# Kernel optimization log

Hardware: AMD Instinct MI355X
Metric: run time of the kernel (lower is better)

Reference implementation:

```python
import jax, jax.numpy as jnp
import numpy as np

N = 50000      # nodes
E = 800000     # edges (before self loops)
IN_D = 128
HID = 128
OUT_D = 64
HEADS = 4
FH = HID // HEADS  # per-head feature dim
NEG_SLOPE = 0.2


def setup_inputs() -> dict:
    key = jax.random.key(0)
    ks = jax.random.split(key, 16)
    s = 0.05
    inp = {
        "x": jax.random.normal(ks[0], (N, IN_D), dtype=jnp.float32),
        "edge_index": jax.random.randint(ks[1], (2, E), 0, N, dtype=jnp.int32),
        "Wi": jax.random.normal(ks[2], (IN_D, HID), dtype=jnp.float32) * s,
        "bi": jnp.zeros((HID,), dtype=jnp.float32),
        "W0": jax.random.normal(ks[3], (HID, HID), dtype=jnp.float32) * s,
        "as0": jax.random.normal(ks[4], (HEADS, FH), dtype=jnp.float32) * s,
        "ad0": jax.random.normal(ks[5], (HEADS, FH), dtype=jnp.float32) * s,
        "b0": jnp.zeros((HID,), dtype=jnp.float32),
        "W1": jax.random.normal(ks[6], (HID, HID), dtype=jnp.float32) * s,
        "as1": jax.random.normal(ks[7], (HEADS, FH), dtype=jnp.float32) * s,
        "ad1": jax.random.normal(ks[8], (HEADS, FH), dtype=jnp.float32) * s,
        "b1": jnp.zeros((HID,), dtype=jnp.float32),
        "Wo": jax.random.normal(ks[9], (HID, OUT_D), dtype=jnp.float32) * s,
        "bo": jnp.zeros((OUT_D,), dtype=jnp.float32),
    }
    return inp


def _gat_layer(h, src, dst, W, a_src, a_dst, b):
    # h: [N, HID]; src/dst: [E'] (with self loops)
    hp = (h @ W).reshape(N, HEADS, FH)               # projected per-head features
    al_s = jnp.einsum('nhf,hf->nh', hp, a_src)       # [N, H]
    al_d = jnp.einsum('nhf,hf->nh', hp, a_dst)
    e = jax.nn.leaky_relu(al_s[src] + al_d[dst], NEG_SLOPE)  # [E', H]
    # neighbor softmax over incoming edges of each dst node (stable)
    m = jax.ops.segment_max(e, dst, num_segments=N)
    m = jnp.where(jnp.isfinite(m), m, 0.0)
    num = jnp.exp(e - m[dst])
    den = jax.ops.segment_sum(num, dst, num_segments=N)
    coef = num / (den[dst] + 1e-16)                  # [E', H]
    out = jax.ops.segment_sum(coef[:, :, None] * hp[src], dst, num_segments=N)
    return out.reshape(N, HID) + b


def reference(x, edge_index, Wi, bi, W0, as0, ad0, b0, W1, as1, ad1, b1, Wo, bo):
    # add self loops (PyG GATConv default)
    loop = jnp.arange(N, dtype=edge_index.dtype)
    src = jnp.concatenate([edge_index[0], loop])
    dst = jnp.concatenate([edge_index[1], loop])

    h = jax.nn.relu(x @ Wi + bi)
    # layer 0 (dropout = identity in eval)
    h = h + jax.nn.relu(_gat_layer(h, src, dst, W0, as0, ad0, b0))
    # layer 1
    h = h + jax.nn.relu(_gat_layer(h, src, dst, W1, as1, ad1, b1))
    return h @ Wo + bo
```

## Files before the change

### kernel.cpp

```cpp
#include <hip/hip_runtime.h>
#include <hip/hip_bf16.h>


__device__ __forceinline__ float lrelu(float x){ return x > 0.f ? x : 0.2f * x; }

typedef __attribute__((ext_vector_type(8))) short bf16x8;
typedef __attribute__((ext_vector_type(8))) char  i8x8;
typedef __attribute__((ext_vector_type(4))) float f32x4;

__device__ __forceinline__ ushort f2bf(float f){
    union { __hip_bfloat16 b; ushort u; } cv;
    cv.b = __float2bfloat16(f);
    return cv.u;
}
__device__ __forceinline__ float bf2f(short u){
    union { uint i; float f; } c;
    c.i = ((uint)(ushort)u) << 16;
    return c.f;
}

constexpr int CAP = 64;
constexpr int BUCKET_CAP = 8192;
constexpr int P1_EDGES = 2048;

__global__ __launch_bounds__(256) void bin_edges_kernel(
    const int* __restrict__ ei, int* __restrict__ gcur, int2* __restrict__ binned, int E, int N)
{
    __shared__ int hist[256], offs[256], gpos[256];
    __shared__ int2 stag[P1_EDGES];
    __shared__ int wsum[4];
    int tid = threadIdx.x;
    hist[tid] = 0;
    __syncthreads();

    int base = blockIdx.x * P1_EDGES;
    int srcv[8], dstv[8], rk[8];
    #pragma unroll
    for (int j = 0; j < 8; j++){
        int e = base + j * 256 + tid;
        if (e < E + N){
            int s, d;
            if (e < E){ s = ei[e]; d = ei[E + e]; } else { s = e - E; d = s; }
            srcv[j] = s; dstv[j] = d;
            rk[j] = atomicAdd(&hist[d >> 8], 1);
        } else dstv[j] = -1;
    }
    __syncthreads();

    int lane = tid & 63, wid = tid >> 6;
    int v = hist[tid];
    int x = v;
    #pragma unroll
    for (int o = 1; o < 64; o <<= 1){ int t = __shfl_up(x, o); if (lane >= o) x += t; }
    if (lane == 63) wsum[wid] = x;
    __syncthreads();
    int woff = 0;
    for (int w2 = 0; w2 < wid; w2++) woff += wsum[w2];
    offs[tid] = woff + x - v;
    __syncthreads();

    #pragma unroll
    for (int j = 0; j < 8; j++){
        if (dstv[j] >= 0){
            int b = dstv[j] >> 8;
            stag[offs[b] + rk[j]] = make_int2(srcv[j], dstv[j]);
        }
    }
    if (hist[tid] > 0) gpos[tid] = atomicAdd(&gcur[tid], hist[tid]);
    __syncthreads();

    int nE = offs[255] + hist[255];
    for (int i = tid; i < nE; i += 256){
        int2 p = stag[i];
        int b = p.y >> 8;
        int idx = gpos[b] + (i - offs[b]);
        if (idx < BUCKET_CAP) binned[(size_t)b * BUCKET_CAP + idx] = p;
    }
}

__global__ __launch_bounds__(256) void build_slots_kernel(
    const int* __restrict__ gcur, const int2* __restrict__ binned,
    int* __restrict__ cnt, int* __restrict__ slots, int N)
{
    __shared__ int cnt_l[256];
    __shared__ int slots_l[256][CAP];
    int tid = threadIdx.x;
    int b = blockIdx.x;
    cnt_l[tid] = 0;
    __syncthreads();

    int ne = gcur[b]; if (ne > BUCKET_CAP) ne = BUCKET_CAP;
    const int2* bp = binned + (size_t)b * BUCKET_CAP;
    for (int i = tid; i < ne; i += 256){
        int2 p = bp[i];
        int ld = p.y & 255;
        int pos = atomicAdd(&cnt_l[ld], 1);
        if (pos < CAP) slots_l[ld][pos] = p.x;
    }
    __syncthreads();

    int node = b * 256 + tid;
    if (node < N) cnt[node] = min(cnt_l[tid], CAP);
    for (int j = tid; j < 256 * CAP; j += 256){
        int n2 = b * 256 + (j >> 6);
        if (n2 < N) slots[(size_t)n2 * CAP + (j & 63)] = slots_l[j >> 6][j & 63];
    }
}

__global__ void wcast_all_kernel(const float* __restrict__ Wi, const float* __restrict__ W0,
                                 const float* __restrict__ W1, const float* __restrict__ Wo,
                                 ushort* __restrict__ ti, ushort* __restrict__ t0,
                                 ushort* __restrict__ t1, ushort* __restrict__ to_){
    int i = blockIdx.x * 256 + threadIdx.x;
    if (i < 16384){
        int k = i >> 7, n = i & 127;        ti[n * 128 + k] = f2bf(Wi[i]);
    } else if (i < 32768){
        int j = i - 16384; int k = j >> 7, n = j & 127;  t0[n * 128 + k] = f2bf(W0[j]);
    } else if (i < 49152){
        int j = i - 32768; int k = j >> 7, n = j & 127;  t1[n * 128 + k] = f2bf(W1[j]);
    } else if (i < 57344){
        int j = i - 49152; int k = j / 64, n = j % 64;   to_[n * 128 + k] = f2bf(Wo[j]);
    }
}

template<int NCOL, bool RELU, bool BIAS, int OUTMODE, bool LOGITS, bool ABF16>
__global__ __launch_bounds__(256) void mfma_matmul_kernel(
    const void* __restrict__ Av,
    const ushort* __restrict__ Wt,
    const float* __restrict__ bias,
    void* __restrict__ Cv,
    float* __restrict__ scales,
    const float* __restrict__ as_, const float* __restrict__ ad_,
    float* __restrict__ als, float* __restrict__ ald, int M)
{
    constexpr int NT = NCOL / 16;
    __shared__ ushort Ws[NCOL][136];
    int tid = threadIdx.x;
    for (int i = tid * 8; i < NCOL * 128; i += 256 * 8){
        int r = i >> 7, c = i & 127;
        *(uint4*)&Ws[r][c] = *(const uint4*)&Wt[i];
    }
    __syncthreads();

    int lane = tid & 63, wave = tid >> 6;
    int r15 = lane & 15;
    int ko  = (lane >> 4) * 8;
    int row  = blockIdx.x * 64 + wave * 16 + r15;
    int rowc = row < M ? row : M - 1;

    f32x4 acc[NT];
    #pragma unroll
    for (int t = 0; t < NT; t++) acc[t] = (f32x4){0.f, 0.f, 0.f, 0.f};

    #pragma unroll
    for (int kt = 0; kt < 4; ++kt){
        bf16x8 af;
        if (ABF16){
            af = *(const bf16x8*)&((const ushort*)Av)[(size_t)rowc * 128 + kt * 32 + ko];
        } else {
            const float* Arow = (const float*)Av + (size_t)rowc * 128;
            float4 a0 = *(const float4*)&Arow[kt * 32 + ko];
            float4 a1 = *(const float4*)&Arow[kt * 32 + ko + 4];
            af[0] = f2bf(a0.x); af[1] = f2bf(a0.y); af[2] = f2bf(a0.z); af[3] = f2bf(a0.w);
            af[4] = f2bf(a1.x); af[5] = f2bf(a1.y); af[6] = f2bf(a1.z); af[7] = f2bf(a1.w);
        }
        #pragma unroll
        for (int t = 0; t < NT; t++){
            bf16x8 bf = *(const bf16x8*)&Ws[t * 16 + r15][kt * 32 + ko];
            acc[t] = __builtin_amdgcn_mfma_f32_16x16x32_bf16(af, bf, acc[t], 0, 0, 0);
        }
    }

    int oc    = lane & 15;
    int orow0 = blockIdx.x * 64 + wave * 16 + (lane >> 4) * 4;

    if (OUTMODE == 2){
        float inv[4], scl[4];
        #pragma unroll
        for (int rg = 0; rg < 4; rg++){
            float m = 0.f;
            #pragma unroll
            for (int t = 0; t < NT; t++) m = fmaxf(m, fabsf(acc[t][rg]));
            #pragma unroll
            for (int o = 1; o < 16; o <<= 1) m = fmaxf(m, __shfl_xor(m, o));
            m = fmaxf(m, 1e-8f);
            scl[rg] = m * (1.f / 127.f);
            inv[rg] = 127.f / m;
        }
        if (oc == 0){
            #pragma unroll
            for (int rg = 0; rg < 4; rg++){
                int orow = orow0 + rg;
                if (orow < M) scales[orow] = scl[rg];
            }
        }
        #pragma unroll
        for (int t = 0; t < NT; t++){
            #pragma unroll
            for (int rg = 0; rg < 4; rg++){
                int orow = orow0 + rg;
                if (orow < M){
                    int q = __float2int_rn(acc[t][rg] * inv[rg]);
                    q = q > 127 ? 127 : (q < -127 ? -127 : q);
                    ((signed char*)Cv)[(size_t)orow * NCOL + t * 16 + oc] = (signed char)q;
                }
            }
        }
    } else {
        #pragma unroll
        for (int t = 0; t < NT; t++){
            int ocol = t * 16 + oc;
            float bv = BIAS ? bias[ocol] : 0.f;
            #pragma unroll
            for (int rg = 0; rg < 4; rg++){
                int orow = orow0 + rg;
                if (orow < M){
                    float v = acc[t][rg] + bv;
                    if (RELU) v = fmaxf(v, 0.f);
                    if (OUTMODE == 1) ((ushort*)Cv)[(size_t)orow * NCOL + ocol] = f2bf(v);
                    else              ((float*)Cv) [(size_t)orow * NCOL + ocol] = v;
                }
            }
        }
    }

    if (LOGITS){
        float sva[4][4], svd[4][4];
        #pragma unroll
        for (int hh = 0; hh < 4; hh++){
            float as0v = as_[hh*32 + oc],      ad0v = ad_[hh*32 + oc];
            float as1v = as_[hh*32 + 16 + oc], ad1v = ad_[hh*32 + 16 + oc];
            #pragma unroll
            for (int rg = 0; rg < 4; rg++){
                sva[hh][rg] = acc[2*hh][rg] * as0v + acc[2*hh+1][rg] * as1v;
                svd[hh][rg] = acc[2*hh][rg] * ad0v + acc[2*hh+1][rg] * ad1v;
            }
        }
        #pragma unroll
        for (int o = 1; o < 16; o <<= 1){
            #pragma unroll
            for (int hh = 0; hh < 4; hh++)
                #pragma unroll
                for (int rg = 0; rg < 4; rg++){
                    sva[hh][rg] += __shfl_xor(sva[hh][rg], o);
                    svd[hh][rg] += __shfl_xor(svd[hh][rg], o);
                }
        }
        if (oc < 4){
            #pragma unroll
            for (int rg = 0; rg < 4; rg++){
                int orow = orow0 + rg;
                if (orow < M){
                    float va = (oc & 2) ? ((oc & 1) ? sva[3][rg] : sva[2][rg])
                                        : ((oc & 1) ? sva[1][rg] : sva[0][rg]);
                    float vd = (oc & 2) ? ((oc & 1) ? svd[3][rg] : svd[2][rg])
                                        : ((oc & 1) ? svd[1][rg] : svd[0][rg]);
                    als[orow * 4 + oc] = va;
                    ald[orow * 4 + oc] = vd;
                }
            }
        }
    }
}

__global__ __launch_bounds__(256) void gat_aggregate_kernel(
    const int* __restrict__ cnt, const int* __restrict__ slots,
    const signed char* __restrict__ hp, const float* __restrict__ scales,
    const float* __restrict__ als, const float* __restrict__ ald,
    const float* __restrict__ bias, ushort* __restrict__ h, int n)
{
    __shared__ float num_s[4][CAP * 5];
    __shared__ float scl_s[4][CAP];
    __shared__ int   src_s[4][CAP];
    int wid = threadIdx.x >> 6;
    int lane = threadIdx.x & 63;
    int node = blockIdx.x * 4 + wid;
    float* nums = num_s[wid];
    float* scls = scl_s[wid];
    int*   srcs = src_s[wid];

    int er = lane >> 4;
    int fg = (lane & 15) * 8;
    int head = (lane & 15) >> 2;
    int f2 = fg + er * 2;

    int deg = 0;
    float4 aldv = make_float4(0.f,0.f,0.f,0.f);
    float hold0 = 0.f, hold1 = 0.f;
    float bv0 = 0.f, bv1 = 0.f;
    if (node < n){
        deg = cnt[node];
        if (deg > CAP) deg = CAP;
        aldv = *(const float4*)&ald[node * 4];
        ushort2 h16 = *(const ushort2*)&h[(size_t)node * 128 + f2];
        hold0 = bf2f(h16.x); hold1 = bf2f(h16.y);
        bv0 = bias[f2]; bv1 = bias[f2 + 1];
    }

    float d0=0.f,d1=0.f,d2=0.f,d3=0.f;
    if (lane < deg){
        int s = slots[node * CAP + lane];
        srcs[lane] = s;
        scls[lane] = scales[s];
        float4 av = *(const float4*)&als[s * 4];
        d0 = __expf(lrelu(av.x + aldv.x));
        d1 = __expf(lrelu(av.y + aldv.y));
        d2 = __expf(lrelu(av.z + aldv.z));
        d3 = __expf(lrelu(av.w + aldv.w));
    }
    float s0=d0, s1=d1, s2=d2, s3=d3;
    #pragma unroll
    for (int o = 1; o < 64; o <<= 1){
        s0+=__shfl_xor(s0,o); s1+=__shfl_xor(s1,o);
        s2+=__shfl_xor(s2,o); s3+=__shfl_xor(s3,o);
    }
    float inv0=1.f/(s0+1e-16f), inv1=1.f/(s1+1e-16f);
    float inv2=1.f/(s2+1e-16f), inv3=1.f/(s3+1e-16f);
    if (lane < deg){
        nums[lane*5+0]=d0*inv0; nums[lane*5+1]=d1*inv1;
        nums[lane*5+2]=d2*inv2; nums[lane*5+3]=d3*inv3;
    }

    float a0=0.f,a1=0.f,a2=0.f,a3=0.f,a4=0.f,a5=0.f,a6=0.f,a7=0.f;
    for (int i = 0; i < deg; i += 8){
        int e0 = i + er, e1 = i + 4 + er;
        bool v0 = e0 < deg, v1 = e1 < deg;
        int ec0 = v0 ? e0 : 0, ec1 = v1 ? e1 : 0;
        int sA = srcs[ec0], sB = srcs[ec1];
        float c0 = nums[ec0*5 + head] * scls[ec0]; c0 = v0 ? c0 : 0.f;
        float c1 = nums[ec1*5 + head] * scls[ec1]; c1 = v1 ? c1 : 0.f;
        i8x8 h0 = *(const i8x8*)&hp[(size_t)sA * 128 + fg];
        i8x8 h1 = *(const i8x8*)&hp[(size_t)sB * 128 + fg];
        a0 = fmaf(c0, (float)h0[0], a0); a1 = fmaf(c0, (float)h0[1], a1);
        a2 = fmaf(c0, (float)h0[2], a2); a3 = fmaf(c0, (float)h0[3], a3);
        a4 = fmaf(c0, (float)h0[4], a4); a5 = fmaf(c0, (float)h0[5], a5);
        a6 = fmaf(c0, (float)h0[6], a6); a7 = fmaf(c0, (float)h0[7], a7);
        a0 = fmaf(c1, (float)h1[0], a0); a1 = fmaf(c1, (float)h1[1], a1);
        a2 = fmaf(c1, (float)h1[2], a2); a3 = fmaf(c1, (float)h1[3], a3);
        a4 = fmaf(c1, (float)h1[4], a4); a5 = fmaf(c1, (float)h1[5], a5);
        a6 = fmaf(c1, (float)h1[6], a6); a7 = fmaf(c1, (float)h1[7], a7);
    }
    a0 += __shfl_xor(a0,16); a0 += __shfl_xor(a0,32);
    a1 += __shfl_xor(a1,16); a1 += __shfl_xor(a1,32);
    a2 += __shfl_xor(a2,16); a2 += __shfl_xor(a2,32);
    a3 += __shfl_xor(a3,16); a3 += __shfl_xor(a3,32);
    a4 += __shfl_xor(a4,16); a4 += __shfl_xor(a4,32);
    a5 += __shfl_xor(a5,16); a5 += __shfl_xor(a5,32);
    a6 += __shfl_xor(a6,16); a6 += __shfl_xor(a6,32);
    a7 += __shfl_xor(a7,16); a7 += __shfl_xor(a7,32);

    if (node < n){
        float sA = (er & 2) ? ((er & 1) ? a6 : a4) : ((er & 1) ? a2 : a0);
        float sB = (er & 2) ? ((er & 1) ? a7 : a5) : ((er & 1) ? a3 : a1);
        float r0 = hold0 + fmaxf(sA + bv0, 0.f);
        float r1 = hold1 + fmaxf(sB + bv1, 0.f);
        ushort2 o2; o2.x = f2bf(r0); o2.y = f2bf(r1);
        *(ushort2*)&h[(size_t)node * 128 + f2] = o2;
    }
}

extern "C" void kernel_launch(void* const* d_in, const int* in_sizes, int n_in,
                              void* d_out, int out_size, void* d_ws, size_t ws_size,
                              hipStream_t stream)
{
    const float* x   = (const float*)d_in[0];
    const int*   ei  = (const int*)d_in[1];
    const float* Wi  = (const float*)d_in[2];
    const float* bi  = (const float*)d_in[3];
    const float* W0  = (const float*)d_in[4];
    const float* as0 = (const float*)d_in[5];
    const float* ad0 = (const float*)d_in[6];
    const float* b0  = (const float*)d_in[7];
    const float* W1  = (const float*)d_in[8];
    const float* as1 = (const float*)d_in[9];
    const float* ad1 = (const float*)d_in[10];
    const float* b1  = (const float*)d_in[11];
    const float* Wo  = (const float*)d_in[12];
    const float* bo  = (const float*)d_in[13];
    float* out = (float*)d_out;

    int N = in_sizes[0] / 128;
    int E = in_sizes[1] / 2;
    int EN = E + N;
    int NB = (N + 255) >> 8;

    char* w = (char*)d_ws;
    ushort* h     = (ushort*)w;      w += (size_t)N * 128 * 2;
    signed char* hpq = (signed char*)w; w += (size_t)N * 128;
    w = (char*)(((uintptr_t)w + 255) & ~(uintptr_t)255);
    float*  scales= (float*)w;       w += (size_t)N * 4;
    float*  als   = (float*)w;       w += (size_t)N * 4 * 4;
    float*  ald   = (float*)w;       w += (size_t)N * 4 * 4;
    int*    cnt   = (int*)w;         w += (size_t)N * 4;
    w = (char*)(((uintptr_t)w + 255) & ~(uintptr_t)255);
    int*    slots = (int*)w;         w += (size_t)N * CAP * 4;
    w = (char*)(((uintptr_t)w + 255) & ~(uintptr_t)255);
    int*    gcur  = (int*)w;         w += 256 * 4;
    w = (char*)(((uintptr_t)w + 255) & ~(uintptr_t)255);
    int2*   binned= (int2*)w;        w += (size_t)NB * BUCKET_CAP * 8;
    w = (char*)(((uintptr_t)w + 255) & ~(uintptr_t)255);
    ushort* wt_i  = (ushort*)w;      w += (size_t)128 * 128 * 2;
    ushort* wt_0  = (ushort*)w;      w += (size_t)128 * 128 * 2;
    ushort* wt_1  = (ushort*)w;      w += (size_t)128 * 128 * 2;
    ushort* wt_o  = (ushort*)w;      w += (size_t)64  * 128 * 2;

    hipMemsetAsync(gcur, 0, 256 * 4, stream);
    bin_edges_kernel<<<(EN + P1_EDGES - 1) / P1_EDGES, 256, 0, stream>>>(ei, gcur, binned, E, N);
    build_slots_kernel<<<NB, 256, 0, stream>>>(gcur, binned, cnt, slots, N);

    wcast_all_kernel<<<224, 256, 0, stream>>>(Wi, W0, W1, Wo, wt_i, wt_0, wt_1, wt_o);

    int mgrid = (N + 63) / 64;
    int agrid = (N + 3) / 4;

    mfma_matmul_kernel<128, true, true, 1, false, false><<<mgrid, 256, 0, stream>>>(
        x, wt_i, bi, h, nullptr, nullptr, nullptr, nullptr, nullptr, N);

    mfma_matmul_kernel<128, false, false, 2, true, true><<<mgrid, 256, 0, stream>>>(
        h, wt_0, nullptr, hpq, scales, as0, ad0, als, ald, N);
    gat_aggregate_kernel<<<agrid, 256, 0, stream>>>(cnt, slots, hpq, scales, als, ald, b0, h, N);

    mfma_matmul_kernel<128, false, false, 2, true, true><<<mgrid, 256, 0, stream>>>(
        h, wt_1, nullptr, hpq, scales, as1, ad1, als, ald, N);
    gat_aggregate_kernel<<<agrid, 256, 0, stream>>>(cnt, slots, hpq, scales, als, ald, b1, h, N);

    mfma_matmul_kernel<64, false, true, 0, false, true><<<mgrid, 256, 0, stream>>>(
        h, wt_o, bo, out, nullptr, nullptr, nullptr, nullptr, nullptr, N);
}
```

Measured before the change: 159.2 us.

## Fuse input projection with layer-0 projection and fold memset into weight cast

The input linear layer (x@Wi+bi, ReLU) and the layer-0 projection with int8 quantization and attention logits now run in one kernel. The intermediate h tile stays in shared memory, which removes one launch and the global re-read of h. The hipMemsetAsync of the bin counters moves into the weight-cast kernel, which now runs first. The fused kernel uses more shared memory (two tiles) and reloads the weights between the two GEMMs, which may lower occupancy.

```diff
diff --git a/kernel.cpp b/kernel.cpp
--- a/kernel.cpp
+++ b/kernel.cpp
@@ -110,8 +110,10 @@
 __global__ void wcast_all_kernel(const float* __restrict__ Wi, const float* __restrict__ W0,
                                  const float* __restrict__ W1, const float* __restrict__ Wo,
                                  ushort* __restrict__ ti, ushort* __restrict__ t0,
-                                 ushort* __restrict__ t1, ushort* __restrict__ to_){
+                                 ushort* __restrict__ t1, ushort* __restrict__ to_,
+                                 int* __restrict__ gcur){
     int i = blockIdx.x * 256 + threadIdx.x;
+    if (blockIdx.x == 0) gcur[threadIdx.x] = 0;
     if (i < 16384){
         int k = i >> 7, n = i & 127;        ti[n * 128 + k] = f2bf(Wi[i]);
     } else if (i < 32768){
@@ -123,9 +125,165 @@
     }
 }
 
-template<int NCOL, bool RELU, bool BIAS, int OUTMODE, bool LOGITS, bool ABF16>
+template<int NT>
+__device__ __forceinline__ void epi_int8(
+    const f32x4* acc, signed char* Cv, float* scales, int oc, int orow0, int M, int NCOL)
+{
+    float inv[4], scl[4];
+    #pragma unroll
+    for (int rg = 0; rg < 4; rg++){
+        float m = 0.f;
+        #pragma unroll
+        for (int t = 0; t < NT; t++) m = fmaxf(m, fabsf(acc[t][rg]));
+        #pragma unroll
+        for (int o = 1; o < 16; o <<= 1) m = fmaxf(m, __shfl_xor(m, o));
+        m = fmaxf(m, 1e-8f);
+        scl[rg] = m * (1.f / 127.f);
+        inv[rg] = 127.f / m;
+    }
+    if (oc == 0){
+        #pragma unroll
+        for (int rg = 0; rg < 4; rg++){
+            int orow = orow0 + rg;
+            if (orow < M) scales[orow] = scl[rg];
+        }
+    }
+    #pragma unroll
+    for (int t = 0; t < NT; t++){
+        #pragma unroll
+        for (int rg = 0; rg < 4; rg++){
+            int orow = orow0 + rg;
+            if (orow < M){
+                int q = __float2int_rn(acc[t][rg] * inv[rg]);
+                q = q > 127 ? 127 : (q < -127 ? -127 : q);
+                Cv[(size_t)orow * NCOL + t * 16 + oc] = (signed char)q;
+            }
+        }
+    }
+}
+
+__device__ __forceinline__ void epi_logits(
+    const f32x4* acc, const float* as_, const float* ad_,
+    float* als, float* ald, int oc, int orow0, int M)
+{
+    float sva[4][4], svd[4][4];
+    #pragma unroll
+    for (int hh = 0; hh < 4; hh++){
+        float as0v = as_[hh*32 + oc],      ad0v = ad_[hh*32 + oc];
+        float as1v = as_[hh*32 + 16 + oc], ad1v = ad_[hh*32 + 16 + oc];
+        #pragma unroll
+        for (int rg = 0; rg < 4; rg++){
+            sva[hh][rg] = acc[2*hh][rg] * as0v + acc[2*hh+1][rg] * as1v;
+            svd[hh][rg] = acc[2*hh][rg] * ad0v + acc[2*hh+1][rg] * ad1v;
+        }
+    }
+    #pragma unroll
+    for (int o = 1; o < 16; o <<= 1){
+        #pragma unroll
+        for (int hh = 0; hh < 4; hh++)
+            #pragma unroll
+            for (int rg = 0; rg < 4; rg++){
+                sva[hh][rg] += __shfl_xor(sva[hh][rg], o);
+                svd[hh][rg] += __shfl_xor(svd[hh][rg], o);
+            }
+    }
+    if (oc < 4){
+        #pragma unroll
+        for (int rg = 0; rg < 4; rg++){
+            int orow = orow0 + rg;
+            if (orow < M){
+                float va = (oc & 2) ? ((oc & 1) ? sva[3][rg] : sva[2][rg])
+                                    : ((oc & 1) ? sva[1][rg] : sva[0][rg]);
+                float vd = (oc & 2) ? ((oc & 1) ? svd[3][rg] : svd[2][rg])
+                                    : ((oc & 1) ? svd[1][rg] : svd[0][rg]);
+                als[orow * 4 + oc] = va;
+                ald[orow * 4 + oc] = vd;
+            }
+        }
+    }
+}
+
+__global__ __launch_bounds__(256) void fused_proj_kernel(
+    const float* __restrict__ x, const ushort* __restrict__ wti, const float* __restrict__ bi,
+    const ushort* __restrict__ wt0, ushort* __restrict__ hout,
+    signed char* __restrict__ hpq, float* __restrict__ scales,
+    const float* __restrict__ as_, const float* __restrict__ ad_,
+    float* __restrict__ als, float* __restrict__ ald, int M)
+{
+    __shared__ ushort Ws[128][136];
+    __shared__ ushort Hs[64][136];
+    int tid = threadIdx.x;
+    for (int i = tid * 8; i < 128 * 128; i += 256 * 8){
+        int r = i >> 7, c = i & 127;
+        *(uint4*)&Ws[r][c] = *(const uint4*)&wti[i];
+    }
+    __syncthreads();
+
+    int lane = tid & 63, wave = tid >> 6;
+    int r15 = lane & 15;
+    int ko  = (lane >> 4) * 8;
+    int row  = blockIdx.x * 64 + wave * 16 + r15;
+    int rowc = row < M ? row : M - 1;
+    const float* Arow = x + (size_t)rowc * 128;
+
+    f32x4 acc[8];
+    #pragma unroll
+    for (int t = 0; t < 8; t++) acc[t] = (f32x4){0.f, 0.f, 0.f, 0.f};
+    #pragma unroll
+    for (int kt = 0; kt < 4; ++kt){
+        float4 a0 = *(const float4*)&Arow[kt * 32 + ko];
+        float4 a1 = *(const float4*)&Arow[kt * 32 + ko + 4];
+        bf16x8 af;
+        af[0] = f2bf(a0.x); af[1] = f2bf(a0.y); af[2] = f2bf(a0.z); af[3] = f2bf(a0.w);
+        af[4] = f2bf(a1.x); af[5] = f2bf(a1.y); af[6] = f2bf(a1.z); af[7] = f2bf(a1.w);
+        #pragma unroll
+        for (int t = 0; t < 8; t++){
+            bf16x8 bf = *(const bf16x8*)&Ws[t * 16 + r15][kt * 32 + ko];
+            acc[t] = __builtin_amdgcn_mfma_f32_16x16x32_bf16(af, bf, acc[t], 0, 0, 0);
+        }
+    }
+    int oc     = lane & 15;
+    int olocal = wave * 16 + (lane >> 4) * 4;
+    int orow0  = blockIdx.x * 64 + olocal;
+    #pragma unroll
+    for (int t = 0; t < 8; t++){
+        int ocol = t * 16 + oc;
+        float bv = bi[ocol];
+        #pragma unroll
+        for (int rg = 0; rg < 4; rg++){
+            float v = fmaxf(acc[t][rg] + bv, 0.f);
+            ushort hv = f2bf(v);
+            Hs[olocal + rg][ocol] = hv;
+            int orow = orow0 + rg;
+            if (orow < M) hout[(size_t)orow * 128 + ocol] = hv;
+        }
+    }
+    __syncthreads();
+
+    for (int i = tid * 8; i < 128 * 128; i += 256 * 8){
+        int r = i >> 7, c = i & 127;
+        *(uint4*)&Ws[r][c] = *(const uint4*)&wt0[i];
+    }
+    __syncthreads();
+
+    #pragma unroll
+    for (int t = 0; t < 8; t++) acc[t] = (f32x4){0.f, 0.f, 0.f, 0.f};
+    #pragma unroll
+    for (int kt = 0; kt < 4; ++kt){
+        bf16x8 af = *(const bf16x8*)&Hs[wave * 16 + r15][kt * 32 + ko];
+        #pragma unroll
+        for (int t = 0; t < 8; t++){
+            bf16x8 bf = *(const bf16x8*)&Ws[t * 16 + r15][kt * 32 + ko];
+            acc[t] = __builtin_amdgcn_mfma_f32_16x16x32_bf16(af, bf, acc[t], 0, 0, 0);
+        }
+    }
+    epi_int8<8>(acc, hpq, scales, oc, orow0, M, 128);
+    epi_logits(acc, as_, ad_, als, ald, oc, orow0, M);
+}
+
+template<int NCOL, int OUTMODE, bool LOGITS>
 __global__ __launch_bounds__(256) void mfma_matmul_kernel(
-    const void* __restrict__ Av,
+    const ushort* __restrict__ A,
     const ushort* __restrict__ Wt,
     const float* __restrict__ bias,
     void* __restrict__ Cv,
@@ -154,16 +312,7 @@
 
     #pragma unroll
     for (int kt = 0; kt < 4; ++kt){
-        bf16x8 af;
-        if (ABF16){
-            af = *(const bf16x8*)&((const ushort*)Av)[(size_t)rowc * 128 + kt * 32 + ko];
-        } else {
-            const float* Arow = (const float*)Av + (size_t)rowc * 128;
-            float4 a0 = *(const float4*)&Arow[kt * 32 + ko];
-            float4 a1 = *(const float4*)&Arow[kt * 32 + ko + 4];
-            af[0] = f2bf(a0.x); af[1] = f2bf(a0.y); af[2] = f2bf(a0.z); af[3] = f2bf(a0.w);
-            af[4] = f2bf(a1.x); af[5] = f2bf(a1.y); af[6] = f2bf(a1.z); af[7] = f2bf(a1.w);
-        }
+        bf16x8 af = *(const bf16x8*)&A[(size_t)rowc * 128 + kt * 32 + ko];
         #pragma unroll
         for (int t = 0; t < NT; t++){
             bf16x8 bf = *(const bf16x8*)&Ws[t * 16 + r15][kt * 32 + ko];
@@ -175,92 +324,20 @@
     int orow0 = blockIdx.x * 64 + wave * 16 + (lane >> 4) * 4;
 
     if (OUTMODE == 2){
-        float inv[4], scl[4];
-        #pragma unroll
-        for (int rg = 0; rg < 4; rg++){
-            float m = 0.f;
-            #pragma unroll
-            for (int t = 0; t < NT; t++) m = fmaxf(m, fabsf(acc[t][rg]));
-            #pragma unroll
-            for (int o = 1; o < 16; o <<= 1) m = fmaxf(m, __shfl_xor(m, o));
-            m = fmaxf(m, 1e-8f);
-            scl[rg] = m * (1.f / 127.f);
-            inv[rg] = 127.f / m;
-        }
-        if (oc == 0){
+        epi_int8<NT>(acc, (signed char*)Cv, scales, oc, orow0, M, NCOL);
+    } else {
+        #pragma unroll
+        for (int t = 0; t < NT; t++){
+            int ocol = t * 16 + oc;
+            float bv = bias[ocol];
             #pragma unroll
             for (int rg = 0; rg < 4; rg++){
                 int orow = orow0 + rg;
-                if (orow < M) scales[orow] = scl[rg];
+                if (orow < M) ((float*)Cv)[(size_t)orow * NCOL + ocol] = acc[t][rg] + bv;
             }
         }
-        #pragma unroll
-        for (int t = 0; t < NT; t++){
-            #pragma unroll
-            for (int rg = 0; rg < 4; rg++){
-                int orow = orow0 + rg;
-                if (orow < M){
-                    int q = __float2int_rn(acc[t][rg] * inv[rg]);
-                    q = q > 127 ? 127 : (q < -127 ? -127 : q);
-                    ((signed char*)Cv)[(size_t)orow * NCOL + t * 16 + oc] = (signed char)q;
-                }
-            }
-        }
-    } else {
-        #pragma unroll
-        for (int t = 0; t < NT; t++){
-            int ocol = t * 16 + oc;
-            float bv = BIAS ? bias[ocol] : 0.f;
-            #pragma unroll
-            for (int rg = 0; rg < 4; rg++){
-                int orow = orow0 + rg;
-                if (orow < M){
-                    float v = acc[t][rg] + bv;
-                    if (RELU) v = fmaxf(v, 0.f);
-                    if (OUTMODE == 1) ((ushort*)Cv)[(size_t)orow * NCOL + ocol] = f2bf(v);
-                    else              ((float*)Cv) [(size_t)orow * NCOL + ocol] = v;
-                }
-            }
-        }
-    }
-
-    if (LOGITS){
-        float sva[4][4], svd[4][4];
-        #pragma unroll
-        for (int hh = 0; hh < 4; hh++){
-            float as0v = as_[hh*32 + oc],      ad0v = ad_[hh*32 + oc];
-            float as1v = as_[hh*32 + 16 + oc], ad1v = ad_[hh*32 + 16 + oc];
-            #pragma unroll
-            for (int rg = 0; rg < 4; rg++){
-                sva[hh][rg] = acc[2*hh][rg] * as0v + acc[2*hh+1][rg] * as1v;
-                svd[hh][rg] = acc[2*hh][rg] * ad0v + acc[2*hh+1][rg] * ad1v;
-            }
-        }
-        #pragma unroll
-        for (int o = 1; o < 16; o <<= 1){
-            #pragma unroll
-            for (int hh = 0; hh < 4; hh++)
-                #pragma unroll
-                for (int rg = 0; rg < 4; rg++){
-                    sva[hh][rg] += __shfl_xor(sva[hh][rg], o);
-                    svd[hh][rg] += __shfl_xor(svd[hh][rg], o);
-                }
-        }
-        if (oc < 4){
-            #pragma unroll
-            for (int rg = 0; rg < 4; rg++){
-                int orow = orow0 + rg;
-                if (orow < M){
-                    float va = (oc & 2) ? ((oc & 1) ? sva[3][rg] : sva[2][rg])
-                                        : ((oc & 1) ? sva[1][rg] : sva[0][rg]);
-                    float vd = (oc & 2) ? ((oc & 1) ? svd[3][rg] : svd[2][rg])
-                                        : ((oc & 1) ? svd[1][rg] : svd[0][rg]);
-                    als[orow * 4 + oc] = va;
-                    ald[orow * 4 + oc] = vd;
-                }
-            }
-        }
-    }
+    }
+    if (LOGITS) epi_logits(acc, as_, ad_, als, ald, oc, orow0, M);
 }
 
 __global__ __launch_bounds__(256) void gat_aggregate_kernel(
@@ -404,26 +481,23 @@
     ushort* wt_1  = (ushort*)w;      w += (size_t)128 * 128 * 2;
     ushort* wt_o  = (ushort*)w;      w += (size_t)64  * 128 * 2;
 
-    hipMemsetAsync(gcur, 0, 256 * 4, stream);
+    int mgrid = (N + 63) / 64;
+    int agrid = (N + 3) / 4;
+
+    wcast_all_kernel<<<224, 256, 0, stream>>>(Wi, W0, W1, Wo, wt_i, wt_0, wt_1, wt_o, gcur);
+
     bin_edges_kernel<<<(EN + P1_EDGES - 1) / P1_EDGES, 256, 0, stream>>>(ei, gcur, binned, E, N);
     build_slots_kernel<<<NB, 256, 0, stream>>>(gcur, binned, cnt, slots, N);
 
-    wcast_all_kernel<<<224, 256, 0, stream>>>(Wi, W0, W1, Wo, wt_i, wt_0, wt_1, wt_o);
-
-    int mgrid = (N + 63) / 64;
-    int agrid = (N + 3) / 4;
-
-    mfma_matmul_kernel<128, true, true, 1, false, false><<<mgrid, 256, 0, stream>>>(
-        x, wt_i, bi, h, nullptr, nullptr, nullptr, nullptr, nullptr, N);
-
-    mfma_matmul_kernel<128, false, false, 2, true, true><<<mgrid, 256, 0, stream>>>(
-        h, wt_0, nullptr, hpq, scales, as0, ad0, als, ald, N);
+    fused_proj_kernel<<<mgrid, 256, 0, stream>>>(
+        x, wt_i, bi, wt_0, h, hpq, scales, as0, ad0, als, ald, N);
+
     gat_aggregate_kernel<<<agrid, 256, 0, stream>>>(cnt, slots, hpq, scales, als, ald, b0, h, N);
 
-    mfma_matmul_kernel<128, false, false, 2, true, true><<<mgrid, 256, 0, stream>>>(
+    mfma_matmul_kernel<128, 2, true><<<mgrid, 256, 0, stream>>>(
         h, wt_1, nullptr, hpq, scales, as1, ad1, als, ald, N);
     gat_aggregate_kernel<<<agrid, 256, 0, stream>>>(cnt, slots, hpq, scales, als, ald, b1, h, N);
 
-    mfma_matmul_kernel<64, false, true, 0, false, true><<<mgrid, 256, 0, stream>>>(
+    mfma_matmul_kernel<64, 0, false><<<mgrid, 256, 0, stream>>>(
         h, wt_o, bo, out, nullptr, nullptr, nullptr, nullptr, nullptr, N);
 }
```

Measured after the change: 158.2 us. Within noise of the previous version (-0.6%).
